# Performance work log

Measured on AMD Instinct MI355X. Metric: run time of the kernel, lower is better.

## Reference

```python
import jax, jax.numpy as jnp
import numpy as np

N_EMBED = 8192
EMBED_DIM = 128
BETA = 1.0
DECAY = 0.99
EPS = 1e-5


def l2norm(t, eps=1e-12):
    # matches F.normalize(p=2, dim=-1)
    n = jnp.linalg.norm(t, axis=-1, keepdims=True)
    return t / jnp.maximum(n, eps)


def setup_inputs() -> dict:
    key = jax.random.key(0)
    k1, k2 = jax.random.split(key)
    z = jax.random.normal(k1, (16, 1024, EMBED_DIM), dtype=jnp.float32)
    embedding = l2norm(jax.random.normal(k2, (N_EMBED, EMBED_DIM), dtype=jnp.float32))
    cluster_size = jnp.zeros((N_EMBED,), dtype=jnp.float32)
    embed_avg = embedding.copy()
    return {"z": z, "embedding": embedding, "cluster_size": cluster_size, "embed_avg": embed_avg}


def reference(z, embedding, cluster_size, embed_avg):
    z_input = z
    zn = l2norm(z)
    zf = zn.reshape(-1, EMBED_DIM)  # [N, d]

    # pairwise squared L2 distances to codebook: [N, n_embed]
    d = (jnp.sum(zf * zf, axis=1, keepdims=True)
         + jnp.sum(embedding * embedding, axis=1)
         - 2.0 * jnp.einsum('bd,nd->bn', zf, embedding))
    encoding_indices = jnp.argmin(d, axis=1)  # [N]

    z_q = embedding[encoding_indices].reshape(zn.shape)
    loss = BETA * jnp.mean((jax.lax.stop_gradient(z_q) - zn) ** 2)

    # EMA update (training branch) -- one-hot scatter expressed as segment sums
    bins = jax.ops.segment_sum(jnp.ones_like(encoding_indices, dtype=zf.dtype),
                               encoding_indices, num_segments=N_EMBED)  # [n_embed]
    new_cluster_size = cluster_size * DECAY + (1.0 - DECAY) * bins

    embed_sum = jax.ops.segment_sum(zf, encoding_indices, num_segments=N_EMBED)  # [n_embed, d]
    embed_normalized = l2norm(embed_sum / (bins[:, None] + EPS))
    embed_normalized = jnp.where((bins == 0)[:, None], embedding, embed_normalized)
    new_embed_avg = embed_avg * DECAY + (1.0 - DECAY) * embed_normalized
    new_embedding = l2norm(new_embed_avg)

    # straight-through estimator
    z_q = z_input + jax.lax.stop_gradient(z_q - z_input)
    return z_q, loss, encoding_indices, new_embedding, new_cluster_size, new_embed_avg
```

## Files before the change

### kernel.cpp

```cpp
#include <hip/hip_runtime.h>
#include <hip/hip_bf16.h>

constexpr int NV = 16384;
constexpr int D  = 128;
constexpr int NE = 8192;
constexpr float DECAY = 0.99f;
constexpr float BETA  = 1.0f;
constexpr float EPS   = 1e-5f;
constexpr float LO_SCALE     = 4096.0f;
constexpr float INV_LO_SCALE = 1.0f / 4096.0f;

constexpr float QSCALE = 65536.0f;
constexpr float QOFF   = 98304.0f;

constexpr int Q = 8;
constexpr int CODES_PER_Q = NE / Q;
constexpr int TILE_C = 64;
constexpr int TILES = CODES_PER_Q / TILE_C;
constexpr int BZ = 128;
constexpr int NCAND = Q * 2;

constexpr size_t WS_Z2    = 0;
constexpr size_t WS_E2    = WS_Z2 + (size_t)NV * 128;
constexpr size_t WS_EN2   = WS_E2 + (size_t)NE * 128;
constexpr size_t WS_MINI2 = WS_EN2 + NE;
constexpr size_t WS_BINS  = WS_Z2;
constexpr size_t WS_ESUM  = WS_BINS + NE;
constexpr size_t WS_LPART = WS_ESUM + (size_t)NE * D;

constexpr size_t OUT_ZQ   = 0;
constexpr size_t OUT_LOSS = OUT_ZQ + (size_t)NV*D;
constexpr size_t OUT_IDX  = OUT_LOSS + 1;
constexpr size_t OUT_EMB  = OUT_IDX + NV;
constexpr size_t OUT_CS   = OUT_EMB + (size_t)NE*D;
constexpr size_t OUT_EAVG = OUT_CS + NE;

using half8  = __attribute__((ext_vector_type(8))) _Float16;
using half2v = __attribute__((ext_vector_type(2))) _Float16;
using f32x16 = __attribute__((ext_vector_type(16))) float;

__device__ inline float waveReduceSum(float v) {
    #pragma unroll
    for (int o = 32; o > 0; o >>= 1) v += __shfl_xor(v, o, 64);
    return v;
}
__device__ inline unsigned umin32(unsigned a, unsigned b) { return a < b ? a : b; }
__device__ inline unsigned umax32(unsigned a, unsigned b) { return a > b ? a : b; }

__device__ inline void gload_lds16(const void* g, void* s) {
    __builtin_amdgcn_global_load_lds(
        (const __attribute__((address_space(1))) unsigned int*)g,
        (__attribute__((address_space(3))) unsigned int*)s, 16, 0, 0);
}

__global__ void k_prep(const float* __restrict__ z, const float* __restrict__ emb,
                       _Float16* __restrict__ z2, _Float16* __restrict__ e2h,
                       float* __restrict__ en2) {
    int tid = threadIdx.x;
    int l = tid & 63;
    int g = blockIdx.x * 4 + (tid >> 6);
    bool isZ = g < NV;
    int row = isZ ? g : g - NV;
    const float* src = isZ ? &z[(size_t)row * D] : &emb[(size_t)row * D];

    const float2 v = *reinterpret_cast<const float2*>(&src[l * 2]);
    float s = waveReduceSum(v.x * v.x + v.y * v.y);
    float x0 = v.x, x1 = v.y;
    if (isZ) {
        float inv = 1.0f / fmaxf(sqrtf(s), 1e-12f);
        x0 *= inv; x1 *= inv;
        _Float16 h0 = (_Float16)x0, h1 = (_Float16)x1;
        _Float16 l0 = (_Float16)((x0 - (float)h0) * LO_SCALE);
        _Float16 l1 = (_Float16)((x1 - (float)h1) * LO_SCALE);
        _Float16* zr = &z2[(size_t)row * 256];
        half2v hh = {h0, h1}, lv = {l0, l1};
        *reinterpret_cast<half2v*>(&zr[l * 2])       = hh;
        *reinterpret_cast<half2v*>(&zr[128 + l * 2]) = lv;
    } else {
        if (l == 0) en2[row] = s;
        _Float16 h0 = (_Float16)x0, h1 = (_Float16)x1;
        half2v hh = {h0, h1};
        *reinterpret_cast<half2v*>(&e2h[(size_t)row * 128 + l * 2]) = hh;
    }
}

__global__ __launch_bounds__(256, 2) void k_dist(
        const _Float16* __restrict__ z2, const _Float16* __restrict__ e2h,
        const float* __restrict__ en2, unsigned* __restrict__ minI2) {
    __shared__ _Float16 eb[2][TILE_C * 128];
    __shared__ float c0s[CODES_PER_Q];

    const int tid = threadIdx.x;
    const int w  = tid >> 6;
    const int l  = tid & 63;
    const int cc = l & 31;
    const int gg = l >> 5;
    const int zb = blockIdx.x * BZ;
    const int q  = blockIdx.y;
    const int cbase0 = q * CODES_PER_Q;

    half8 a_h[8], a_l[8];
    {
        const size_t row = (size_t)(zb + w * 32 + cc);
        #pragma unroll
        for (int kf = 0; kf < 8; ++kf) {
            a_h[kf] = *reinterpret_cast<const half8*>(&z2[row * 256 + kf * 16 + gg * 8]);
            a_l[kf] = *reinterpret_cast<const half8*>(&z2[row * 256 + 128 + kf * 16 + gg * 8]);
        }
    }

    for (int i = tid; i < CODES_PER_Q; i += 256)
        c0s[i] = fmaf(en2[cbase0 + i], QSCALE, QOFF);

    int soff[4];
    #pragma unroll
    for (int i = 0; i < 4; ++i) {
        int c = (w * 4 + i) * 64 + l;
        int code = c >> 4, slot = c & 15;
        soff[i] = code * 256 + ((slot ^ (code & 7)) * 16);
    }
    auto stage = [&](int b, int t) {
        const char* tbase = reinterpret_cast<const char*>(&e2h[(size_t)(cbase0 + t * TILE_C) * 128]);
        #pragma unroll
        for (int i = 0; i < 4; ++i)
            gload_lds16(tbase + soff[i], &eb[b][(size_t)(w * 4 + i) * 512]);
    };

    stage(0, 0);

    unsigned bU1[16], bU2[16];
    #pragma unroll
    for (int i = 0; i < 16; ++i) { bU1[i] = 0xFFFFFFFFu; bU2[i] = 0xFFFFFFFFu; }

    const int swz = cc & 7;

    int cur = 0;
    for (int t = 0; t < TILES; ++t) {
        __syncthreads();
        if (t + 1 < TILES) stage(cur ^ 1, t + 1);

        #pragma unroll
        for (int n = 0; n < 2; ++n) {
            const char* rbase = reinterpret_cast<const char*>(&eb[cur][0])
                                + (n * 32 + cc) * 256;
            half8 b0 = *reinterpret_cast<const half8*>(rbase + (((0 * 2 + gg) ^ swz) * 16));
            half8 b1 = *reinterpret_cast<const half8*>(rbase + (((1 * 2 + gg) ^ swz) * 16));
            half8 b2 = *reinterpret_cast<const half8*>(rbase + (((2 * 2 + gg) ^ swz) * 16));
            half8 b3 = *reinterpret_cast<const half8*>(rbase + (((3 * 2 + gg) ^ swz) * 16));
            half8 b4 = *reinterpret_cast<const half8*>(rbase + (((4 * 2 + gg) ^ swz) * 16));
            half8 b5 = *reinterpret_cast<const half8*>(rbase + (((5 * 2 + gg) ^ swz) * 16));
            half8 b6 = *reinterpret_cast<const half8*>(rbase + (((6 * 2 + gg) ^ swz) * 16));
            half8 b7 = *reinterpret_cast<const half8*>(rbase + (((7 * 2 + gg) ^ swz) * 16));

            f32x16 accA1{}, accA2{}, accB1{}, accB2{};
            accA1 = __builtin_amdgcn_mfma_f32_32x32x16_f16(a_h[0], b0, accA1, 0, 0, 0);
            accB1 = __builtin_amdgcn_mfma_f32_32x32x16_f16(a_l[0], b0, accB1, 0, 0, 0);
            accA2 = __builtin_amdgcn_mfma_f32_32x32x16_f16(a_h[4], b4, accA2, 0, 0, 0);
            accB2 = __builtin_amdgcn_mfma_f32_32x32x16_f16(a_l[4], b4, accB2, 0, 0, 0);
            accA1 = __builtin_amdgcn_mfma_f32_32x32x16_f16(a_h[1], b1, accA1, 0, 0, 0);
            accB1 = __builtin_amdgcn_mfma_f32_32x32x16_f16(a_l[1], b1, accB1, 0, 0, 0);
            accA2 = __builtin_amdgcn_mfma_f32_32x32x16_f16(a_h[5], b5, accA2, 0, 0, 0);
            accB2 = __builtin_amdgcn_mfma_f32_32x32x16_f16(a_l[5], b5, accB2, 0, 0, 0);
            accA1 = __builtin_amdgcn_mfma_f32_32x32x16_f16(a_h[2], b2, accA1, 0, 0, 0);
            accB1 = __builtin_amdgcn_mfma_f32_32x32x16_f16(a_l[2], b2, accB1, 0, 0, 0);
            accA2 = __builtin_amdgcn_mfma_f32_32x32x16_f16(a_h[6], b6, accA2, 0, 0, 0);
            accB2 = __builtin_amdgcn_mfma_f32_32x32x16_f16(a_l[6], b6, accB2, 0, 0, 0);
            accA1 = __builtin_amdgcn_mfma_f32_32x32x16_f16(a_h[3], b3, accA1, 0, 0, 0);
            accB1 = __builtin_amdgcn_mfma_f32_32x32x16_f16(a_l[3], b3, accB1, 0, 0, 0);
            accA2 = __builtin_amdgcn_mfma_f32_32x32x16_f16(a_h[7], b7, accA2, 0, 0, 0);
            accB2 = __builtin_amdgcn_mfma_f32_32x32x16_f16(a_l[7], b7, accB2, 0, 0, 0);

            const unsigned code = (unsigned)(cbase0 + t * TILE_C + n * 32 + cc);
            const float c0 = c0s[t * TILE_C + n * 32 + cc];
            #pragma unroll
            for (int r = 0; r < 16; ++r) {
                float sumA = accA1[r] + accA2[r];
                float sumB = accB1[r] + accB2[r];
                float tq = fmaf(-2.0f * QSCALE, sumA, c0);
                tq = fmaf(-2.0f * QSCALE * INV_LO_SCALE, sumB, tq);
                unsigned u = ((unsigned)tq << 13) | code;
                unsigned m1 = bU1[r];
                bU2[r] = umin32(umax32(u, m1), bU2[r]);
                bU1[r] = umin32(u, m1);
            }
        }
        cur ^= 1;
    }

    #pragma unroll
    for (int r = 0; r < 16; ++r) {
        unsigned u1 = bU1[r], u2 = bU2[r];
        #pragma unroll
        for (int m = 1; m < 32; m <<= 1) {
            unsigned o1 = (unsigned)__shfl_xor((int)u1, m, 64);
            unsigned o2 = (unsigned)__shfl_xor((int)u2, m, 64);
            unsigned hi = umax32(u1, o1);
            u1 = umin32(u1, o1);
            u2 = umin32(umin32(u2, o2), hi);
        }
        if (cc == 0) {
            int zrow = zb + w * 32 + (r & 3) + 8 * (r >> 2) + 4 * gg;
            size_t o = ((size_t)zrow * Q + q) * 2;
            minI2[o] = u1; minI2[o + 1] = u2;
        }
    }
}

__global__ void k_gather(const float* __restrict__ z, const float* __restrict__ emb,
                         const float* __restrict__ en2, const unsigned* __restrict__ minI2,
                         float* __restrict__ outZq, float* __restrict__ outIdx,
                         float* __restrict__ bins, float* __restrict__ esum,
                         float* __restrict__ lossPart) {
    __shared__ float zsh[4][128];
    int tid = threadIdx.x;
    int wave = tid >> 6, lane = tid & 63;
    int zr = blockIdx.x * 4 + wave;

    const float2 zv = *reinterpret_cast<const float2*>(&z[(size_t)zr * D + lane * 2]);
    float s = waveReduceSum(zv.x * zv.x + zv.y * zv.y);
    float inv = 1.0f / fmaxf(sqrtf(s), 1e-12f);
    float znx = zv.x * inv, zny = zv.y * inv;
    zsh[wave][lane * 2]     = znx;
    zsh[wave][lane * 2 + 1] = zny;
    __syncthreads();

    float cv = 3.4e38f; int ci = 0x7fffffff;
    if (lane < NCAND) {
        ci = (int)(minI2[(size_t)zr * NCAND + lane] & 8191u);
        const float* er = &emb[(size_t)ci * D];
        float dot = 0.0f;
        #pragma unroll 8
        for (int k = 0; k < 128; ++k) dot = fmaf(zsh[wave][k], er[k], dot);
        cv = fmaf(-2.0f, dot, en2[ci]);
    }
    float bv = cv; int bi = ci;
    #pragma unroll
    for (int m = 1; m < NCAND; m <<= 1) {
        float ov = __shfl_xor(bv, m, 64);
        int   oi = __shfl_xor(bi, m, 64);
        if (ov < bv || (ov == bv && oi < bi)) { bv = ov; bi = oi; }
    }
    bi = __shfl(bi, 0, 64);
    if (lane == 0) outIdx[zr] = (float)bi;

    float2 e = *reinterpret_cast<const float2*>(&emb[(size_t)bi * D + lane * 2]);
    *reinterpret_cast<float2*>(&outZq[(size_t)zr * D + lane * 2]) = e;

    float dx = e.x - znx, dy = e.y - zny;
    float ls = waveReduceSum(dx * dx + dy * dy);

    if (lane == 0) atomicAdd(&bins[bi], 1.0f);
    atomicAdd(&esum[(size_t)bi * D + lane * 2 + 0], znx);
    atomicAdd(&esum[(size_t)bi * D + lane * 2 + 1], zny);

    __shared__ float part[4];
    if (lane == 0) part[wave] = ls;
    __syncthreads();
    if (tid == 0) lossPart[blockIdx.x] = (part[0] + part[1]) + (part[2] + part[3]);
}

__global__ void k_codebook(const float* __restrict__ emb, const float* __restrict__ csz,
                           const float* __restrict__ eavg, const float* __restrict__ bins,
                           const float* __restrict__ esum, const float* __restrict__ lossPart,
                           float* __restrict__ outEmb, float* __restrict__ outCs,
                           float* __restrict__ outEavg, float* __restrict__ outLoss) {
    int tid = threadIdx.x;
    int wave = tid >> 6, lane = tid & 63;
    int n = blockIdx.x * 4 + wave;

    if (blockIdx.x == 0) {
        float s = 0.0f;
        for (int i = tid; i < 4096; i += 256) s += lossPart[i];
        s = waveReduceSum(s);
        __shared__ float p[4];
        if ((tid & 63) == 0) p[tid >> 6] = s;
        __syncthreads();
        if (tid == 0) outLoss[0] = BETA * ((p[0] + p[1]) + (p[2] + p[3])) / (float)((size_t)NV * D);
    }

    float b = bins[n];
    if (lane == 0) outCs[n] = csz[n] * DECAY + (1.0f - DECAY) * b;

    float2 es = *reinterpret_cast<const float2*>(&esum[(size_t)n * D + lane * 2]);
    float invb = 1.0f / (b + EPS);
    float mx = es.x * invb, my = es.y * invb;
    float ss = waveReduceSum(mx * mx + my * my);
    float invn = 1.0f / fmaxf(sqrtf(ss), 1e-12f);

    float2 er = *reinterpret_cast<const float2*>(&emb[(size_t)n * D + lane * 2]);
    float enx = (b == 0.0f) ? er.x : mx * invn;
    float eny = (b == 0.0f) ? er.y : my * invn;

    float2 ea = *reinterpret_cast<const float2*>(&eavg[(size_t)n * D + lane * 2]);
    float nax = ea.x * DECAY + (1.0f - DECAY) * enx;
    float nay = ea.y * DECAY + (1.0f - DECAY) * eny;
    float2 no; no.x = nax; no.y = nay;
    *reinterpret_cast<float2*>(&outEavg[(size_t)n * D + lane * 2]) = no;

    float ss2 = waveReduceSum(nax * nax + nay * nay);
    float inv2 = 1.0f / fmaxf(sqrtf(ss2), 1e-12f);
    float2 ne; ne.x = nax * inv2; ne.y = nay * inv2;
    *reinterpret_cast<float2*>(&outEmb[(size_t)n * D + lane * 2]) = ne;
}

extern "C" void kernel_launch(void* const* d_in, const int* in_sizes, int n_in,
                              void* d_out, int out_size, void* d_ws, size_t ws_size,
                              hipStream_t stream) {
    (void)in_sizes; (void)n_in; (void)out_size; (void)ws_size;
    const float* z    = (const float*)d_in[0];
    const float* emb  = (const float*)d_in[1];
    const float* csz  = (const float*)d_in[2];
    const float* eavg = (const float*)d_in[3];
    float* out = (float*)d_out;
    float* ws  = (float*)d_ws;

    _Float16* z2   = (_Float16*)(ws + WS_Z2);
    _Float16* e2h  = (_Float16*)(ws + WS_E2);
    float*    en2  = ws + WS_EN2;
    unsigned* minI2 = (unsigned*)(ws + WS_MINI2);
    float*  bins   = ws + WS_BINS;
    float*  esum   = ws + WS_ESUM;
    float*  lpart  = ws + WS_LPART;

    k_prep<<<(NV + NE) / 4, 256, 0, stream>>>(z, emb, z2, e2h, en2);
    k_dist<<<dim3(NV / BZ, Q), 256, 0, stream>>>(z2, e2h, en2, minI2);
    hipMemsetAsync(bins, 0, ((size_t)NE + (size_t)NE * D) * sizeof(float), stream);
    k_gather<<<NV / 4, 256, 0, stream>>>(z, emb, en2, minI2,
                                         out + OUT_ZQ, out + OUT_IDX, bins, esum, lpart);
    k_codebook<<<NE / 4, 256, 0, stream>>>(emb, csz, eavg, bins, esum, lpart,
                                           out + OUT_EMB, out + OUT_CS, out + OUT_EAVG,
                                           out + OUT_LOSS);
}
```

Baseline: 153.3 us.

## Give each wave private LDS codebook tiles and stage gather candidates through LDS

Measured after the change: 142.6 us. 6.9% less time.

```diff
diff --git a/kernel.cpp b/kernel.cpp
--- a/kernel.cpp
+++ b/kernel.cpp
@@ -13,10 +13,10 @@
 constexpr float QSCALE = 65536.0f;
 constexpr float QOFF   = 98304.0f;
 
-constexpr int Q = 8;
+constexpr int Q = 4;
 constexpr int CODES_PER_Q = NE / Q;
-constexpr int TILE_C = 64;
-constexpr int TILES = CODES_PER_Q / TILE_C;
+constexpr int SUBT = 32;
+constexpr int TILES = CODES_PER_Q / SUBT;
 constexpr int BZ = 128;
 constexpr int NCAND = Q * 2;
 
@@ -87,7 +87,7 @@
 __global__ __launch_bounds__(256, 2) void k_dist(
         const _Float16* __restrict__ z2, const _Float16* __restrict__ e2h,
         const float* __restrict__ en2, unsigned* __restrict__ minI2) {
-    __shared__ _Float16 eb[2][TILE_C * 128];
+    __shared__ _Float16 eb[4][2][SUBT * 128];
     __shared__ float c0s[CODES_PER_Q];
 
     const int tid = threadIdx.x;
@@ -111,19 +111,20 @@
 
     for (int i = tid; i < CODES_PER_Q; i += 256)
         c0s[i] = fmaf(en2[cbase0 + i], QSCALE, QOFF);
-
-    int soff[4];
-    #pragma unroll
-    for (int i = 0; i < 4; ++i) {
-        int c = (w * 4 + i) * 64 + l;
+    __syncthreads();
+
+    int soff[8];
+    #pragma unroll
+    for (int i = 0; i < 8; ++i) {
+        int c = i * 64 + l;
         int code = c >> 4, slot = c & 15;
         soff[i] = code * 256 + ((slot ^ (code & 7)) * 16);
     }
     auto stage = [&](int b, int t) {
-        const char* tbase = reinterpret_cast<const char*>(&e2h[(size_t)(cbase0 + t * TILE_C) * 128]);
+        const char* tbase = reinterpret_cast<const char*>(&e2h[(size_t)(cbase0 + t * SUBT) * 128]);
         #pragma unroll
-        for (int i = 0; i < 4; ++i)
-            gload_lds16(tbase + soff[i], &eb[b][(size_t)(w * 4 + i) * 512]);
+        for (int i = 0; i < 8; ++i)
+            gload_lds16(tbase + soff[i], &eb[w][b][(size_t)i * 512]);
     };
 
     stage(0, 0);
@@ -136,53 +137,54 @@
 
     int cur = 0;
     for (int t = 0; t < TILES; ++t) {
-        __syncthreads();
-        if (t + 1 < TILES) stage(cur ^ 1, t + 1);
-
+        if (t + 1 < TILES) {
+            stage(cur ^ 1, t + 1);
+            asm volatile("s_waitcnt vmcnt(8)" ::: "memory");
+        } else {
+            asm volatile("s_waitcnt vmcnt(0)" ::: "memory");
+        }
+        __builtin_amdgcn_sched_barrier(0);
+
+        const char* rbase = reinterpret_cast<const char*>(&eb[w][cur][0]) + cc * 256;
+        half8 b0 = *reinterpret_cast<const half8*>(rbase + (((0 * 2 + gg) ^ swz) * 16));
+        half8 b1 = *reinterpret_cast<const half8*>(rbase + (((1 * 2 + gg) ^ swz) * 16));
+        half8 b2 = *reinterpret_cast<const half8*>(rbase + (((2 * 2 + gg) ^ swz) * 16));
+        half8 b3 = *reinterpret_cast<const half8*>(rbase + (((3 * 2 + gg) ^ swz) * 16));
+        half8 b4 = *reinterpret_cast<const half8*>(rbase + (((4 * 2 + gg) ^ swz) * 16));
+        half8 b5 = *reinterpret_cast<const half8*>(rbase + (((5 * 2 + gg) ^ swz) * 16));
+        half8 b6 = *reinterpret_cast<const half8*>(rbase + (((6 * 2 + gg) ^ swz) * 16));
+        half8 b7 = *reinterpret_cast<const half8*>(rbase + (((7 * 2 + gg) ^ swz) * 16));
+
+        f32x16 accA1{}, accA2{}, accB1{}, accB2{};
+        accA1 = __builtin_amdgcn_mfma_f32_32x32x16_f16(a_h[0], b0, accA1, 0, 0, 0);
+        accB1 = __builtin_amdgcn_mfma_f32_32x32x16_f16(a_l[0], b0, accB1, 0, 0, 0);
+        accA2 = __builtin_amdgcn_mfma_f32_32x32x16_f16(a_h[4], b4, accA2, 0, 0, 0);
+        accB2 = __builtin_amdgcn_mfma_f32_32x32x16_f16(a_l[4], b4, accB2, 0, 0, 0);
+        accA1 = __builtin_amdgcn_mfma_f32_32x32x16_f16(a_h[1], b1, accA1, 0, 0, 0);
+        accB1 = __builtin_amdgcn_mfma_f32_32x32x16_f16(a_l[1], b1, accB1, 0, 0, 0);
+        accA2 = __builtin_amdgcn_mfma_f32_32x32x16_f16(a_h[5], b5, accA2, 0, 0, 0);
+        accB2 = __builtin_amdgcn_mfma_f32_32x32x16_f16(a_l[5], b5, accB2, 0, 0, 0);
+        accA1 = __builtin_amdgcn_mfma_f32_32x32x16_f16(a_h[2], b2, accA1, 0, 0, 0);
+        accB1 = __builtin_amdgcn_mfma_f32_32x32x16_f16(a_l[2], b2, accB1, 0, 0, 0);
+        accA2 = __builtin_amdgcn_mfma_f32_32x32x16_f16(a_h[6], b6, accA2, 0, 0, 0);
+        accB2 = __builtin_amdgcn_mfma_f32_32x32x16_f16(a_l[6], b6, accB2, 0, 0, 0);
+        accA1 = __builtin_amdgcn_mfma_f32_32x32x16_f16(a_h[3], b3, accA1, 0, 0, 0);
+        accB1 = __builtin_amdgcn_mfma_f32_32x32x16_f16(a_l[3], b3, accB1, 0, 0, 0);
+        accA2 = __builtin_amdgcn_mfma_f32_32x32x16_f16(a_h[7], b7, accA2, 0, 0, 0);
+        accB2 = __builtin_amdgcn_mfma_f32_32x32x16_f16(a_l[7], b7, accB2, 0, 0, 0);
+
+        const unsigned code = (unsigned)(cbase0 + t * SUBT + cc);
+        const float c0 = c0s[t * SUBT + cc];
         #pragma unroll
-        for (int n = 0; n < 2; ++n) {
-            const char* rbase = reinterpret_cast<const char*>(&eb[cur][0])
-                                + (n * 32 + cc) * 256;
-            half8 b0 = *reinterpret_cast<const half8*>(rbase + (((0 * 2 + gg) ^ swz) * 16));
-            half8 b1 = *reinterpret_cast<const half8*>(rbase + (((1 * 2 + gg) ^ swz) * 16));
-            half8 b2 = *reinterpret_cast<const half8*>(rbase + (((2 * 2 + gg) ^ swz) * 16));
-            half8 b3 = *reinterpret_cast<const half8*>(rbase + (((3 * 2 + gg) ^ swz) * 16));
-            half8 b4 = *reinterpret_cast<const half8*>(rbase + (((4 * 2 + gg) ^ swz) * 16));
-            half8 b5 = *reinterpret_cast<const half8*>(rbase + (((5 * 2 + gg) ^ swz) * 16));
-            half8 b6 = *reinterpret_cast<const half8*>(rbase + (((6 * 2 + gg) ^ swz) * 16));
-            half8 b7 = *reinterpret_cast<const half8*>(rbase + (((7 * 2 + gg) ^ swz) * 16));
-
-            f32x16 accA1{}, accA2{}, accB1{}, accB2{};
-            accA1 = __builtin_amdgcn_mfma_f32_32x32x16_f16(a_h[0], b0, accA1, 0, 0, 0);
-            accB1 = __builtin_amdgcn_mfma_f32_32x32x16_f16(a_l[0], b0, accB1, 0, 0, 0);
-            accA2 = __builtin_amdgcn_mfma_f32_32x32x16_f16(a_h[4], b4, accA2, 0, 0, 0);
-            accB2 = __builtin_amdgcn_mfma_f32_32x32x16_f16(a_l[4], b4, accB2, 0, 0, 0);
-            accA1 = __builtin_amdgcn_mfma_f32_32x32x16_f16(a_h[1], b1, accA1, 0, 0, 0);
-            accB1 = __builtin_amdgcn_mfma_f32_32x32x16_f16(a_l[1], b1, accB1, 0, 0, 0);
-            accA2 = __builtin_amdgcn_mfma_f32_32x32x16_f16(a_h[5], b5, accA2, 0, 0, 0);
-            accB2 = __builtin_amdgcn_mfma_f32_32x32x16_f16(a_l[5], b5, accB2, 0, 0, 0);
-            accA1 = __builtin_amdgcn_mfma_f32_32x32x16_f16(a_h[2], b2, accA1, 0, 0, 0);
-            accB1 = __builtin_amdgcn_mfma_f32_32x32x16_f16(a_l[2], b2, accB1, 0, 0, 0);
-            accA2 = __builtin_amdgcn_mfma_f32_32x32x16_f16(a_h[6], b6, accA2, 0, 0, 0);
-            accB2 = __builtin_amdgcn_mfma_f32_32x32x16_f16(a_l[6], b6, accB2, 0, 0, 0);
-            accA1 = __builtin_amdgcn_mfma_f32_32x32x16_f16(a_h[3], b3, accA1, 0, 0, 0);
-            accB1 = __builtin_amdgcn_mfma_f32_32x32x16_f16(a_l[3], b3, accB1, 0, 0, 0);
-            accA2 = __builtin_amdgcn_mfma_f32_32x32x16_f16(a_h[7], b7, accA2, 0, 0, 0);
-            accB2 = __builtin_amdgcn_mfma_f32_32x32x16_f16(a_l[7], b7, accB2, 0, 0, 0);
-
-            const unsigned code = (unsigned)(cbase0 + t * TILE_C + n * 32 + cc);
-            const float c0 = c0s[t * TILE_C + n * 32 + cc];
-            #pragma unroll
-            for (int r = 0; r < 16; ++r) {
-                float sumA = accA1[r] + accA2[r];
-                float sumB = accB1[r] + accB2[r];
-                float tq = fmaf(-2.0f * QSCALE, sumA, c0);
-                tq = fmaf(-2.0f * QSCALE * INV_LO_SCALE, sumB, tq);
-                unsigned u = ((unsigned)tq << 13) | code;
-                unsigned m1 = bU1[r];
-                bU2[r] = umin32(umax32(u, m1), bU2[r]);
-                bU1[r] = umin32(u, m1);
-            }
+        for (int r = 0; r < 16; ++r) {
+            float sumA = accA1[r] + accA2[r];
+            float sumB = accB1[r] + accB2[r];
+            float tq = fmaf(-2.0f * QSCALE, sumA, c0);
+            tq = fmaf(-2.0f * QSCALE * INV_LO_SCALE, sumB, tq);
+            unsigned u = ((unsigned)tq << 13) | code;
+            unsigned m1 = bU1[r];
+            bU2[r] = umin32(umax32(u, m1), bU2[r]);
+            bU1[r] = umin32(u, m1);
         }
         cur ^= 1;
     }
@@ -212,6 +214,7 @@
                          float* __restrict__ bins, float* __restrict__ esum,
                          float* __restrict__ lossPart) {
     __shared__ float zsh[4][128];
+    __shared__ float ecs[4][NCAND][132];
     int tid = threadIdx.x;
     int wave = tid >> 6, lane = tid & 63;
     int zr = blockIdx.x * 4 + wave;
@@ -222,15 +225,22 @@
     float znx = zv.x * inv, zny = zv.y * inv;
     zsh[wave][lane * 2]     = znx;
     zsh[wave][lane * 2 + 1] = zny;
-    __syncthreads();
-
-    float cv = 3.4e38f; int ci = 0x7fffffff;
+
+    int ci = 0x7fffffff;
+    if (lane < NCAND) ci = (int)(minI2[(size_t)zr * NCAND + lane] & 8191u);
+    #pragma unroll
+    for (int c = 0; c < NCAND; ++c) {
+        int cc_ = __shfl(ci, c, 64);
+        const float2 ev = *reinterpret_cast<const float2*>(&emb[(size_t)cc_ * D + lane * 2]);
+        ecs[wave][c][lane * 2]     = ev.x;
+        ecs[wave][c][lane * 2 + 1] = ev.y;
+    }
+
+    float cv = 3.4e38f;
     if (lane < NCAND) {
-        ci = (int)(minI2[(size_t)zr * NCAND + lane] & 8191u);
-        const float* er = &emb[(size_t)ci * D];
         float dot = 0.0f;
         #pragma unroll 8
-        for (int k = 0; k < 128; ++k) dot = fmaf(zsh[wave][k], er[k], dot);
+        for (int k = 0; k < 128; ++k) dot = fmaf(zsh[wave][k], ecs[wave][lane][k], dot);
         cv = fmaf(-2.0f, dot, en2[ci]);
     }
     float bv = cv; int bi = ci;
```
